# Kernel tuning notes

Hardware: AMD Instinct MI355X
Metric: run time of the kernel (lower is better)

The kernel has to match this reference:

```python
import jax, jax.numpy as jnp
import numpy as np

E = 16          # num_expert
CAP = 1024


def setup_inputs() -> dict:
    key = jax.random.key(0)
    k1, k2, k3, k4 = jax.random.split(key, 4)
    B, L, D_in, D_out, S = 2, 4096, 1024, 4096, 512
    inp = jax.random.normal(k1, (B, L, D_in), jnp.float32)
    # counts must sum to B*L; use a balanced assignment (tokens pre-sorted by expert)
    fwd_expert_count = jnp.full((E,), (B * L) // E, dtype=jnp.int32)
    weight = jax.random.normal(k2, (E, D_out, D_in), jnp.float32) * (1.0 / np.sqrt(D_in))
    bias = jax.random.normal(k3, (E, D_out), jnp.float32) * 0.02
    components = jax.random.normal(k4, (E, S, D_out), jnp.float32) * (1.0 / np.sqrt(D_out))
    return {"inp": inp, "fwd_expert_count": fwd_expert_count, "weight": weight,
            "bias": bias, "components": components}


def _forward(inp, fwd_expert_count, weight, bias, components):
    flat = inp.reshape(-1, inp.shape[-1])            # [T, D_in]
    T = flat.shape[0]
    n_exp = fwd_expert_count.shape[0]
    counts = fwd_expert_count.astype(jnp.int32)
    # per-token expert id and position within its expert segment (tokens are
    # contiguous per expert, matching fastmoe's dispatch layout)
    expert_ids = jnp.repeat(jnp.arange(n_exp, dtype=jnp.int32), counts,
                            total_repeat_length=T)                    # [T]
    offsets = jnp.concatenate([jnp.zeros((1,), jnp.int32), jnp.cumsum(counts)])
    pos = jnp.arange(T, dtype=jnp.int32) - offsets[expert_ids]        # [T]
    # scatter tokens into a padded [E, CAP, D_in] buffer (static capacity)
    padded = jnp.zeros((n_exp, CAP, flat.shape[-1]), flat.dtype)
    padded = padded.at[expert_ids, pos].set(flat)
    # grouped expert GEMM: y_e = x_e @ W_e^T + b_e  (padded rows never read back)
    y = jnp.einsum('eci,eoi->eco', padded, weight) + bias[:, None, :]  # [E, CAP, D_out]
    # projection onto components (einsum 'nkd,ksd->nks' in padded layout)
    proj = jnp.einsum('ecd,esd->ecs', y, components)                   # [E, CAP, S]
    # gather real tokens back (the upscale_proj branch in the source is dead code:
    # its result is never used in the returned output)
    out = proj[expert_ids, pos]                                        # [T, S]
    return out.reshape(inp.shape[:-1] + (proj.shape[-1],))


def reference(inp, fwd_expert_count, weight, bias, components):
    return _forward(inp, fwd_expert_count, weight, bias, components)
```

## Files before the change

kernel.cpp:

```cpp
#include <hip/hip_runtime.h>


#define NEXP 16
#define TTOK 8192
#define DIN  1024
#define DOUT 4096
#define SDIM 512
#define LDSS 40

typedef short short8 __attribute__((ext_vector_type(8)));
typedef float floatx4 __attribute__((ext_vector_type(4)));
typedef unsigned short ushort_t;

__device__ __forceinline__ ushort_t f2bf(float f) {
    union { float f; unsigned u; } v; v.f = f;
    unsigned r = v.u + 0x7FFFu + ((v.u >> 16) & 1u);
    return (ushort_t)(r >> 16);
}

__device__ __forceinline__ unsigned cvtpk(float lo, float hi) {
    unsigned r;
    asm("v_cvt_pk_bf16_f32 %0, %1, %2" : "=v"(r) : "v"(lo), "v"(hi));
    return r;
}

#define GLL16(g, l) __builtin_amdgcn_global_load_lds( \
    (const __attribute__((address_space(1))) void*)(g), \
    (__attribute__((address_space(3))) void*)(l), 16, 0, 0)

__global__ __launch_bounds__(256)
void cvt_kernel(const float* __restrict__ src, ushort_t* __restrict__ dst, int n8) {
    const int i = blockIdx.x * 256 + threadIdx.x;
    if (i >= n8) return;
    const float4 a = ((const float4*)src)[2 * i];
    const float4 b = ((const float4*)src)[2 * i + 1];
    short8 o;
    o[0] = (short)f2bf(a.x); o[1] = (short)f2bf(a.y);
    o[2] = (short)f2bf(a.z); o[3] = (short)f2bf(a.w);
    o[4] = (short)f2bf(b.x); o[5] = (short)f2bf(b.y);
    o[6] = (short)f2bf(b.z); o[7] = (short)f2bf(b.w);
    ((short8*)dst)[i] = o;
}

template<bool G1>
__global__ __launch_bounds__(512, 2)
void gemm8p(const ushort_t* __restrict__ Ain, const int* __restrict__ counts,
            const float* __restrict__ Bf, const float* __restrict__ bias,
            ushort_t* __restrict__ Yout, float* __restrict__ Pout) {
    __shared__ __align__(16) ushort_t As[2 * 16384];
    __shared__ __align__(16) ushort_t Bs[2 * 16384];

    int e, mt, nt, kq;
    if constexpr (G1) {
        const int l = ((blockIdx.x & 7) << 6) | (blockIdx.x >> 3);
        e = l >> 5; nt = (l >> 1) & 15; mt = l & 1; kq = 0;
    } else {
        const int l = ((blockIdx.x & 7) << 5) | (blockIdx.x >> 3);
        e = l >> 4; kq = (l >> 2) & 3; nt = (l >> 1) & 1; mt = l & 1;
    }
    const int LDK = G1 ? DIN : DOUT;

    int off = 0;
    for (int i = 0; i < e; ++i) off += counts[i];
    const int cnt = counts[e];

    const int tid = threadIdx.x, wave = tid >> 6, lane = tid & 63;
    const int wm = wave >> 2, wn = wave & 3;
    const int l15 = lane & 15, quad = lane >> 4;
    const int srow = (wave << 3) + (lane >> 3);
    const int swz8 = ((lane & 7) ^ (lane >> 3)) << 3;
    const int aseg = off + (mt << 8);

    const ushort_t* ap[4];
    #pragma unroll
    for (int q = 0; q < 4; ++q) {
        int r = aseg + (q << 6) + srow; if (r >= TTOK) r = TTOK - 1;
        ap[q] = Ain + (size_t)r * LDK + (G1 ? 0 : (kq << 10)) + swz8;
    }
    const float* bpq[4];
    {
        const float* Bbase = G1
            ? (Bf + (size_t)e * DOUT * DIN  + ((size_t)(nt << 8)) * DIN)
            : (Bf + (size_t)e * SDIM * DOUT + ((size_t)(nt << 8)) * DOUT + (kq << 10));
        #pragma unroll
        for (int q = 0; q < 4; ++q)
            bpq[q] = Bbase + (size_t)((q << 6) + srow) * LDK + ((lane & 7) << 3);
    }
    const int aLdsW  = (wave << 9);
    const int bWrOff = (srow << 6) + swz8;

    auto rdA = [&](int bufe, int m, int s) -> short8 {
        return *(const short8*)&As[bufe + ((wm << 7) + (m << 4) + l15) * 64
                                   + ((((s << 2) | quad) ^ (lane & 7)) << 3)];
    };
    auto rdB = [&](int bufe, int n, int s) -> short8 {
        return *(const short8*)&Bs[bufe + ((wn << 6) + (n << 4) + l15) * 64
                                   + ((((s << 2) | quad) ^ (lane & 7)) << 3)];
    };

    floatx4 acc[8][4] = {};
    short8 bfv[4][2], af0[2], af1[2];
    float4 bq[4][2];

#define GA(NB, q, kt) GLL16(ap[q] + ((kt) << 6), As + (NB) + ((q) << 12) + aLdsW)
#define LB(q, kt) { const float* _p = bpq[q] + ((kt) << 6); \
    bq[q][0] = *(const float4*)_p; bq[q][1] = *(const float4*)(_p + 4); }
#define WRB(NB, q) { uint4 _w; \
    _w.x = cvtpk(bq[q][0].x, bq[q][0].y); _w.y = cvtpk(bq[q][0].z, bq[q][0].w); \
    _w.z = cvtpk(bq[q][1].x, bq[q][1].y); _w.w = cvtpk(bq[q][1].z, bq[q][1].w); \
    *(uint4*)&Bs[(NB) + ((q) << 12) + bWrOff] = _w; }
#define RDB_ALL(BUFE) { _Pragma("unroll") \
    for (int n = 0; n < 4; ++n) { bfv[n][0] = rdB(BUFE,n,0); bfv[n][1] = rdB(BUFE,n,1); } }
#define RDA2(BUFE, M0) { af0[0]=rdA(BUFE,M0,0); af0[1]=rdA(BUFE,M0,1); \
                         af1[0]=rdA(BUFE,(M0)+1,0); af1[1]=rdA(BUFE,(M0)+1,1); }
#define MFMA16(M0) { \
    __builtin_amdgcn_s_setprio(1); \
    _Pragma("unroll") for (int n = 0; n < 4; ++n) { \
      acc[M0][n]     = __builtin_amdgcn_mfma_f32_16x16x32_bf16(af0[0], bfv[n][0], acc[M0][n],     0,0,0); \
      acc[M0][n]     = __builtin_amdgcn_mfma_f32_16x16x32_bf16(af0[1], bfv[n][1], acc[M0][n],     0,0,0); \
      acc[(M0)+1][n] = __builtin_amdgcn_mfma_f32_16x16x32_bf16(af1[0], bfv[n][0], acc[(M0)+1][n], 0,0,0); \
      acc[(M0)+1][n] = __builtin_amdgcn_mfma_f32_16x16x32_bf16(af1[1], bfv[n][1], acc[(M0)+1][n], 0,0,0); } \
    __builtin_amdgcn_s_setprio(0); }
#define VMC(N) asm volatile("s_waitcnt vmcnt(" #N ")" ::: "memory")
#define LGKM0  asm volatile("s_waitcnt lgkmcnt(0)" ::: "memory")
#define BAR()  __builtin_amdgcn_s_barrier()

#define TILE(BUF, NBUF, KA, KB) { \
    RDB_ALL(BUF); RDA2(BUF, 0); \
    GA(NBUF, 0, KA); GA(NBUF, 1, KA); \
    VMC(6); WRB(NBUF, 0); WRB(NBUF, 1); \
    LGKM0; BAR(); MFMA16(0); BAR(); \
    RDA2(BUF, 2); \
    GA(NBUF, 2, KA); GA(NBUF, 3, KA); \
    VMC(4); WRB(NBUF, 2); WRB(NBUF, 3); \
    LGKM0; BAR(); MFMA16(2); BAR(); \
    RDA2(BUF, 4); \
    LB(0, KB); LB(1, KB); \
    BAR(); MFMA16(4); BAR(); \
    RDA2(BUF, 6); \
    LB(2, KB); LB(3, KB); \
    VMC(8); \
    BAR(); MFMA16(6); BAR(); }

    LB(0, 0); LB(1, 0); LB(2, 0); LB(3, 0);
    GA(0, 0, 0); GA(0, 1, 0); GA(0, 2, 0); GA(0, 3, 0);
    VMC(4);
    WRB(0, 0); WRB(0, 1); WRB(0, 2); WRB(0, 3);
    LB(0, 1); LB(1, 1); LB(2, 1); LB(3, 1);
    VMC(8);
    LGKM0; BAR();

    #pragma unroll 1
    for (int it = 0; it < 8; ++it) {
        const int ka0 = 2 * it + 1;
        const int kb0 = (it < 7) ? 2 * it + 2 : 15;
        const int kb1 = (it < 7) ? 2 * it + 3 : 15;
        TILE(0, 16384, ka0, kb0);
        TILE(16384, 0, kb0, kb1);
    }

#undef TILE
#undef GA
#undef LB
#undef WRB
#undef RDB_ALL
#undef RDA2
#undef MFMA16
#undef VMC
#undef LGKM0
#undef BAR

    if constexpr (G1) {
        float bv[4];
        #pragma unroll
        for (int n = 0; n < 4; ++n)
            bv[n] = bias[e * DOUT + (nt << 8) + (wn << 6) + (n << 4) + l15];
        #pragma unroll
        for (int m = 0; m < 8; ++m) {
            #pragma unroll
            for (int rg = 0; rg < 4; ++rg) {
                const int trow = (mt << 8) + (wm << 7) + (m << 4) + (quad << 2) + rg;
                if (trow < cnt) {
                    ushort_t* yp = Yout + (size_t)(off + trow) * DOUT + (nt << 8) + (wn << 6);
                    #pragma unroll
                    for (int n = 0; n < 4; ++n)
                        yp[(n << 4) + l15] = f2bf(acc[m][n][rg] + bv[n]);
                }
            }
        }
    } else {
        float* pp = Pout + (size_t)kq * ((size_t)TTOK * SDIM);
        #pragma unroll
        for (int m = 0; m < 8; ++m) {
            #pragma unroll
            for (int rg = 0; rg < 4; ++rg) {
                const int trow = (mt << 8) + (wm << 7) + (m << 4) + (quad << 2) + rg;
                if (trow < cnt) {
                    float* op = pp + (size_t)(off + trow) * SDIM + (nt << 8) + (wn << 6);
                    #pragma unroll
                    for (int n = 0; n < 4; ++n)
                        op[(n << 4) + l15] = acc[m][n][rg];
                }
            }
        }
    }
}

__global__ __launch_bounds__(256)
void reduce4_kernel(const float* __restrict__ P, float* __restrict__ O) {
    const int i = blockIdx.x * 256 + threadIdx.x;
    const size_t S = (size_t)TTOK * SDIM;
    const float4 a = ((const float4*)P)[i];
    const float4 b = ((const float4*)(P + S))[i];
    const float4 c = ((const float4*)(P + 2 * S))[i];
    const float4 d = ((const float4*)(P + 3 * S))[i];
    ((float4*)O)[i] = make_float4(a.x + b.x + c.x + d.x, a.y + b.y + c.y + d.y,
                                  a.z + b.z + c.z + d.z, a.w + b.w + c.w + d.w);
}

__global__ __launch_bounds__(256, 2)
void gemm1_o(const float* __restrict__ X, const int* __restrict__ counts,
             const float* __restrict__ W, const float* __restrict__ bias,
             ushort_t* __restrict__ Y) {
    __shared__ __align__(16) ushort_t As[128 * LDSS];
    __shared__ __align__(16) ushort_t Bs[128 * LDSS];
    const int bid = blockIdx.x;
    const int e = bid >> 7, r_ = bid & 127;
    const int n_tile = r_ >> 2, m_tile = r_ & 3;
    int off = 0;
    for (int i = 0; i < e; ++i) off += counts[i];
    const int cnt = counts[e];
    const int t = threadIdx.x, wave = t >> 6, lane = t & 63;
    const int wm = (wave & 1) << 6, wn = (wave >> 1) << 6;
    const int l15 = lane & 15, quad = lane >> 4;
    const float* Wp = W + (size_t)e * DOUT * DIN + (size_t)(n_tile << 7) * DIN;
    floatx4 acc[4][4] = {};
    const int srow = t >> 3, scol = (t & 7) << 2;
    for (int k0 = 0; k0 < DIN; k0 += 32) {
        #pragma unroll
        for (int p = 0; p < 4; ++p) {
            const int row = srow + (p << 5);
            int grow = off + (m_tile << 7) + row;
            if (grow >= TTOK) grow = 0;
            const float4 v = *(const float4*)(X + (size_t)grow * DIN + k0 + scol);
            unsigned lo = (unsigned)f2bf(v.x) | ((unsigned)f2bf(v.y) << 16);
            unsigned hi = (unsigned)f2bf(v.z) | ((unsigned)f2bf(v.w) << 16);
            *(uint2*)&As[row * LDSS + scol] = make_uint2(lo, hi);
        }
        #pragma unroll
        for (int p = 0; p < 4; ++p) {
            const int row = srow + (p << 5);
            const float4 v = *(const float4*)(Wp + (size_t)row * DIN + k0 + scol);
            unsigned lo = (unsigned)f2bf(v.x) | ((unsigned)f2bf(v.y) << 16);
            unsigned hi = (unsigned)f2bf(v.z) | ((unsigned)f2bf(v.w) << 16);
            *(uint2*)&Bs[row * LDSS + scol] = make_uint2(lo, hi);
        }
        __syncthreads();
        short8 af[4], bfr[4];
        #pragma unroll
        for (int i = 0; i < 4; ++i) {
            af[i]  = *(const short8*)&As[(wm + (i << 4) + l15) * LDSS + (quad << 3)];
            bfr[i] = *(const short8*)&Bs[(wn + (i << 4) + l15) * LDSS + (quad << 3)];
        }
        #pragma unroll
        for (int mi = 0; mi < 4; ++mi)
            #pragma unroll
            for (int ni = 0; ni < 4; ++ni)
                acc[mi][ni] = __builtin_amdgcn_mfma_f32_16x16x32_bf16(
                    af[mi], bfr[ni], acc[mi][ni], 0, 0, 0);
        __syncthreads();
    }
    float bv[4];
    #pragma unroll
    for (int ni = 0; ni < 4; ++ni)
        bv[ni] = bias[e * DOUT + (n_tile << 7) + wn + (ni << 4) + l15];
    #pragma unroll
    for (int mi = 0; mi < 4; ++mi)
        #pragma unroll
        for (int rg = 0; rg < 4; ++rg) {
            const int trow = (m_tile << 7) + wm + (mi << 4) + (quad << 2) + rg;
            if (trow < cnt) {
                ushort_t* yp = Y + (size_t)(off + trow) * DOUT + (n_tile << 7) + wn;
                #pragma unroll
                for (int ni = 0; ni < 4; ++ni)
                    yp[(ni << 4) + l15] = f2bf(acc[mi][ni][rg] + bv[ni]);
            }
        }
}

__global__ __launch_bounds__(256, 2)
void gemm2_o(const ushort_t* __restrict__ Y, const int* __restrict__ counts,
             const float* __restrict__ C, float* __restrict__ O) {
    __shared__ __align__(16) ushort_t As[128 * LDSS];
    __shared__ __align__(16) ushort_t Bs[128 * LDSS];
    const int bid = blockIdx.x;
    const int e = bid >> 4, r_ = bid & 15;
    const int n_tile = r_ >> 2, m_tile = r_ & 3;
    int off = 0;
    for (int i = 0; i < e; ++i) off += counts[i];
    const int cnt = counts[e];
    const int t = threadIdx.x, wave = t >> 6, lane = t & 63;
    const int wm = (wave & 1) << 6, wn = (wave >> 1) << 6;
    const int l15 = lane & 15, quad = lane >> 4;
    const float* Cp = C + (size_t)e * SDIM * DOUT + (size_t)(n_tile << 7) * DOUT;
    floatx4 acc[4][4] = {};
    const int arow = t >> 2, achk = (t & 3) << 3;
    const int srow = t >> 3, scol = (t & 7) << 2;
    for (int k0 = 0; k0 < DOUT; k0 += 32) {
        #pragma unroll
        for (int p = 0; p < 2; ++p) {
            const int row = arow + (p << 6);
            int grow = off + (m_tile << 7) + row;
            if (grow >= TTOK) grow = 0;
            const short8 v = *(const short8*)(Y + (size_t)grow * DOUT + k0 + achk);
            *(short8*)&As[row * LDSS + achk] = v;
        }
        #pragma unroll
        for (int p = 0; p < 4; ++p) {
            const int row = srow + (p << 5);
            const float4 v = *(const float4*)(Cp + (size_t)row * DOUT + k0 + scol);
            unsigned lo = (unsigned)f2bf(v.x) | ((unsigned)f2bf(v.y) << 16);
            unsigned hi = (unsigned)f2bf(v.z) | ((unsigned)f2bf(v.w) << 16);
            *(uint2*)&Bs[row * LDSS + scol] = make_uint2(lo, hi);
        }
        __syncthreads();
        short8 af[4], bfr[4];
        #pragma unroll
        for (int i = 0; i < 4; ++i) {
            af[i]  = *(const short8*)&As[(wm + (i << 4) + l15) * LDSS + (quad << 3)];
            bfr[i] = *(const short8*)&Bs[(wn + (i << 4) + l15) * LDSS + (quad << 3)];
        }
        #pragma unroll
        for (int mi = 0; mi < 4; ++mi)
            #pragma unroll
            for (int ni = 0; ni < 4; ++ni)
                acc[mi][ni] = __builtin_amdgcn_mfma_f32_16x16x32_bf16(
                    af[mi], bfr[ni], acc[mi][ni], 0, 0, 0);
        __syncthreads();
    }
    #pragma unroll
    for (int mi = 0; mi < 4; ++mi)
        #pragma unroll
        for (int rg = 0; rg < 4; ++rg) {
            const int trow = (m_tile << 7) + wm + (mi << 4) + (quad << 2) + rg;
            if (trow < cnt) {
                float* op = O + (size_t)(off + trow) * SDIM + (n_tile << 7) + wn;
                #pragma unroll
                for (int ni = 0; ni < 4; ++ni)
                    op[(ni << 4) + l15] = acc[mi][ni][rg];
            }
        }
}

extern "C" void kernel_launch(void* const* d_in, const int* in_sizes, int n_in,
                              void* d_out, int out_size, void* d_ws, size_t ws_size,
                              hipStream_t stream) {
    const float* X      = (const float*)d_in[0];
    const int*   counts = (const int*)d_in[1];
    const float* W      = (const float*)d_in[2];
    const float* bias   = (const float*)d_in[3];
    const float* comp   = (const float*)d_in[4];
    float* out = (float*)d_out;

    const size_t OFF_XB = 0;
    const size_t OFF_Y  = 16777216;
    const size_t OFF_P  = 83886080;
    const size_t NEED   = 150994944;

    if (ws_size >= NEED) {
        ushort_t* Xb = (ushort_t*)((char*)d_ws + OFF_XB);
        ushort_t* Y  = (ushort_t*)((char*)d_ws + OFF_Y);
        float*    P  = (float*)((char*)d_ws + OFF_P);

        cvt_kernel<<<dim3(4096), dim3(256), 0, stream>>>(X, Xb, 1048576);
        gemm8p<true><<<dim3(512),  dim3(512), 0, stream>>>(Xb, counts, W, bias, Y, nullptr);
        gemm8p<false><<<dim3(256), dim3(512), 0, stream>>>(Y, counts, comp, nullptr, nullptr, P);
        reduce4_kernel<<<dim3(4096), dim3(256), 0, stream>>>(P, out);
    } else {
        ushort_t* Y = (ushort_t*)d_ws;
        gemm1_o<<<dim3(2048), dim3(256), 0, stream>>>(X, counts, W, bias, Y);
        gemm2_o<<<dim3(256),  dim3(256), 0, stream>>>(Y, counts, comp, out);
    }
}
```

Measured before the change: 566.3 us.

## Retile second GEMM to split-K by 2 with narrower N tiles

The second GEMM now splits K into 2 chunks of 2048 instead of 4 chunks of 1024, and uses 128-wide N tiles instead of 256-wide ones, with a dedicated kernel and a half-size B buffer in LDS. The partial-sum buffer shrinks from 4 to 2 slices, so the reduction kernel reads half as much data and the workspace requirement drops. The trade-off is a longer K loop per block and lower MFMA work per A-tile load, because the same A tile is now reused across fewer N columns.

```diff
diff --git a/kernel.cpp b/kernel.cpp
--- a/kernel.cpp
+++ b/kernel.cpp
@@ -42,23 +42,20 @@
     ((short8*)dst)[i] = o;
 }
 
-template<bool G1>
+#define VMC(N) asm volatile("s_waitcnt vmcnt(" #N ")" ::: "memory")
+#define LGKM0  asm volatile("s_waitcnt lgkmcnt(0)" ::: "memory")
+#define BAR()  __builtin_amdgcn_s_barrier()
+
 __global__ __launch_bounds__(512, 2)
-void gemm8p(const ushort_t* __restrict__ Ain, const int* __restrict__ counts,
-            const float* __restrict__ Bf, const float* __restrict__ bias,
-            ushort_t* __restrict__ Yout, float* __restrict__ Pout) {
+void gemm1_8p(const ushort_t* __restrict__ Ain, const int* __restrict__ counts,
+              const float* __restrict__ Bf, const float* __restrict__ bias,
+              ushort_t* __restrict__ Yout) {
     __shared__ __align__(16) ushort_t As[2 * 16384];
     __shared__ __align__(16) ushort_t Bs[2 * 16384];
 
-    int e, mt, nt, kq;
-    if constexpr (G1) {
-        const int l = ((blockIdx.x & 7) << 6) | (blockIdx.x >> 3);
-        e = l >> 5; nt = (l >> 1) & 15; mt = l & 1; kq = 0;
-    } else {
-        const int l = ((blockIdx.x & 7) << 5) | (blockIdx.x >> 3);
-        e = l >> 4; kq = (l >> 2) & 3; nt = (l >> 1) & 1; mt = l & 1;
-    }
-    const int LDK = G1 ? DIN : DOUT;
+    const int l = ((blockIdx.x & 7) << 6) | (blockIdx.x >> 3);
+    const int e = l >> 5;
+    const int nt = (l >> 1) & 15, mt = l & 1;
 
     int off = 0;
     for (int i = 0; i < e; ++i) off += counts[i];
@@ -75,16 +72,14 @@
     #pragma unroll
     for (int q = 0; q < 4; ++q) {
         int r = aseg + (q << 6) + srow; if (r >= TTOK) r = TTOK - 1;
-        ap[q] = Ain + (size_t)r * LDK + (G1 ? 0 : (kq << 10)) + swz8;
+        ap[q] = Ain + (size_t)r * DIN + swz8;
     }
     const float* bpq[4];
     {
-        const float* Bbase = G1
-            ? (Bf + (size_t)e * DOUT * DIN  + ((size_t)(nt << 8)) * DIN)
-            : (Bf + (size_t)e * SDIM * DOUT + ((size_t)(nt << 8)) * DOUT + (kq << 10));
+        const float* Bbase = Bf + (size_t)e * DOUT * DIN + ((size_t)(nt << 8)) * DIN;
         #pragma unroll
         for (int q = 0; q < 4; ++q)
-            bpq[q] = Bbase + (size_t)((q << 6) + srow) * LDK + ((lane & 7) << 3);
+            bpq[q] = Bbase + (size_t)((q << 6) + srow) * DIN + ((lane & 7) << 3);
     }
     const int aLdsW  = (wave << 9);
     const int bWrOff = (srow << 6) + swz8;
@@ -121,11 +116,8 @@
       acc[(M0)+1][n] = __builtin_amdgcn_mfma_f32_16x16x32_bf16(af1[0], bfv[n][0], acc[(M0)+1][n], 0,0,0); \
       acc[(M0)+1][n] = __builtin_amdgcn_mfma_f32_16x16x32_bf16(af1[1], bfv[n][1], acc[(M0)+1][n], 0,0,0); } \
     __builtin_amdgcn_s_setprio(0); }
-#define VMC(N) asm volatile("s_waitcnt vmcnt(" #N ")" ::: "memory")
-#define LGKM0  asm volatile("s_waitcnt lgkmcnt(0)" ::: "memory")
-#define BAR()  __builtin_amdgcn_s_barrier()
-
-#define TILE(BUF, NBUF, KA, KB) { \
+
+#define TILE1(BUF, NBUF, KA, KB) { \
     RDB_ALL(BUF); RDA2(BUF, 0); \
     GA(NBUF, 0, KA); GA(NBUF, 1, KA); \
     VMC(6); WRB(NBUF, 0); WRB(NBUF, 1); \
@@ -155,67 +147,175 @@
         const int ka0 = 2 * it + 1;
         const int kb0 = (it < 7) ? 2 * it + 2 : 15;
         const int kb1 = (it < 7) ? 2 * it + 3 : 15;
-        TILE(0, 16384, ka0, kb0);
-        TILE(16384, 0, kb0, kb1);
-    }
-
-#undef TILE
+        TILE1(0, 16384, ka0, kb0);
+        TILE1(16384, 0, kb0, kb1);
+    }
+    asm volatile("s_waitcnt vmcnt(0)" ::: "memory");
+
+#undef TILE1
 #undef GA
 #undef LB
 #undef WRB
 #undef RDB_ALL
 #undef RDA2
 #undef MFMA16
-#undef VMC
-#undef LGKM0
-#undef BAR
-
-    if constexpr (G1) {
-        float bv[4];
-        #pragma unroll
-        for (int n = 0; n < 4; ++n)
-            bv[n] = bias[e * DOUT + (nt << 8) + (wn << 6) + (n << 4) + l15];
-        #pragma unroll
-        for (int m = 0; m < 8; ++m) {
-            #pragma unroll
-            for (int rg = 0; rg < 4; ++rg) {
-                const int trow = (mt << 8) + (wm << 7) + (m << 4) + (quad << 2) + rg;
-                if (trow < cnt) {
-                    ushort_t* yp = Yout + (size_t)(off + trow) * DOUT + (nt << 8) + (wn << 6);
-                    #pragma unroll
-                    for (int n = 0; n < 4; ++n)
-                        yp[(n << 4) + l15] = f2bf(acc[m][n][rg] + bv[n]);
-                }
+
+    float bv[4];
+    #pragma unroll
+    for (int n = 0; n < 4; ++n)
+        bv[n] = bias[e * DOUT + (nt << 8) + (wn << 6) + (n << 4) + l15];
+    #pragma unroll
+    for (int m = 0; m < 8; ++m) {
+        #pragma unroll
+        for (int rg = 0; rg < 4; ++rg) {
+            const int trow = (mt << 8) + (wm << 7) + (m << 4) + (quad << 2) + rg;
+            if (trow < cnt) {
+                ushort_t* yp = Yout + (size_t)(off + trow) * DOUT + (nt << 8) + (wn << 6);
+                #pragma unroll
+                for (int n = 0; n < 4; ++n)
+                    yp[(n << 4) + l15] = f2bf(acc[m][n][rg] + bv[n]);
             }
         }
-    } else {
-        float* pp = Pout + (size_t)kq * ((size_t)TTOK * SDIM);
-        #pragma unroll
-        for (int m = 0; m < 8; ++m) {
-            #pragma unroll
-            for (int rg = 0; rg < 4; ++rg) {
-                const int trow = (mt << 8) + (wm << 7) + (m << 4) + (quad << 2) + rg;
-                if (trow < cnt) {
-                    float* op = pp + (size_t)(off + trow) * SDIM + (nt << 8) + (wn << 6);
-                    #pragma unroll
-                    for (int n = 0; n < 4; ++n)
-                        op[(n << 4) + l15] = acc[m][n][rg];
-                }
+    }
+}
+
+__global__ __launch_bounds__(512, 2)
+void gemm2_8p(const ushort_t* __restrict__ Yin, const int* __restrict__ counts,
+              const float* __restrict__ comp, float* __restrict__ P) {
+    __shared__ __align__(16) ushort_t As[2 * 16384];
+    __shared__ __align__(16) ushort_t Bs[2 * 8192];
+
+    const int l = ((blockIdx.x & 7) << 5) | (blockIdx.x >> 3);
+    const int e = l >> 4;
+    const int r = l & 15;
+    const int mt = r & 1, nt2 = (r >> 1) & 3, kq = r >> 3;
+
+    int off = 0;
+    for (int i = 0; i < e; ++i) off += counts[i];
+    const int cnt = counts[e];
+
+    const int tid = threadIdx.x, wave = tid >> 6, lane = tid & 63;
+    const int wm = wave >> 2, wn = wave & 3;
+    const int l15 = lane & 15, quad = lane >> 4;
+    const int srow = (wave << 3) + (lane >> 3);
+    const int swz8 = ((lane & 7) ^ (lane >> 3)) << 3;
+
+    const ushort_t* ap[4];
+    #pragma unroll
+    for (int q = 0; q < 4; ++q) {
+        int rr = off + (mt << 8) + (q << 6) + srow; if (rr >= TTOK) rr = TTOK - 1;
+        ap[q] = Yin + (size_t)rr * DOUT + (kq << 11) + swz8;
+    }
+    const float* bph[2];
+    {
+        const float* Bbase = comp + (size_t)e * SDIM * DOUT
+                           + ((size_t)(nt2 << 7)) * DOUT + (kq << 11);
+        #pragma unroll
+        for (int h = 0; h < 2; ++h)
+            bph[h] = Bbase + (size_t)((h << 6) + srow) * DOUT + ((lane & 7) << 3);
+    }
+    const int aLdsW  = (wave << 9);
+    const int bWrOff = (srow << 6) + swz8;
+
+    auto rdA = [&](int bufe, int m, int s) -> short8 {
+        return *(const short8*)&As[bufe + ((wm << 7) + (m << 4) + l15) * 64
+                                   + ((((s << 2) | quad) ^ (lane & 7)) << 3)];
+    };
+    auto rdB = [&](int bufe, int n, int s) -> short8 {
+        return *(const short8*)&Bs[bufe + ((wn << 5) + (n << 4) + l15) * 64
+                                   + ((((s << 2) | quad) ^ (lane & 7)) << 3)];
+    };
+
+    floatx4 acc[8][2] = {};
+    short8 bfv[2][2], af0[2], af1[2];
+    float4 bq[2][2];
+
+#define GA2(AB, q, kt) GLL16(ap[q] + ((kt) << 6), As + (AB) + ((q) << 12) + aLdsW)
+#define LB2(h, kt) { const float* _p = bph[h] + ((kt) << 6); \
+    bq[h][0] = *(const float4*)_p; bq[h][1] = *(const float4*)(_p + 4); }
+#define WRB2(BB, h) { uint4 _w; \
+    _w.x = cvtpk(bq[h][0].x, bq[h][0].y); _w.y = cvtpk(bq[h][0].z, bq[h][0].w); \
+    _w.z = cvtpk(bq[h][1].x, bq[h][1].y); _w.w = cvtpk(bq[h][1].z, bq[h][1].w); \
+    *(uint4*)&Bs[(BB) + ((h) << 12) + bWrOff] = _w; }
+#define RDB_ALL2(BB) { _Pragma("unroll") \
+    for (int n = 0; n < 2; ++n) { bfv[n][0] = rdB(BB,n,0); bfv[n][1] = rdB(BB,n,1); } }
+#define RDA2(AB, M0) { af0[0]=rdA(AB,M0,0); af0[1]=rdA(AB,M0,1); \
+                       af1[0]=rdA(AB,(M0)+1,0); af1[1]=rdA(AB,(M0)+1,1); }
+#define MFMA8(M0) { \
+    __builtin_amdgcn_s_setprio(1); \
+    _Pragma("unroll") for (int n = 0; n < 2; ++n) { \
+      acc[M0][n]     = __builtin_amdgcn_mfma_f32_16x16x32_bf16(af0[0], bfv[n][0], acc[M0][n],     0,0,0); \
+      acc[M0][n]     = __builtin_amdgcn_mfma_f32_16x16x32_bf16(af0[1], bfv[n][1], acc[M0][n],     0,0,0); \
+      acc[(M0)+1][n] = __builtin_amdgcn_mfma_f32_16x16x32_bf16(af1[0], bfv[n][0], acc[(M0)+1][n], 0,0,0); \
+      acc[(M0)+1][n] = __builtin_amdgcn_mfma_f32_16x16x32_bf16(af1[1], bfv[n][1], acc[(M0)+1][n], 0,0,0); } \
+    __builtin_amdgcn_s_setprio(0); }
+
+#define TILE2(AB, BB, NAB, NBB, KA, KB) { \
+    RDB_ALL2(BB); RDA2(AB, 0); \
+    GA2(NAB, 0, KA); GA2(NAB, 1, KA); \
+    VMC(4); WRB2(NBB, 0); \
+    LGKM0; BAR(); MFMA8(0); BAR(); \
+    RDA2(AB, 2); \
+    GA2(NAB, 2, KA); GA2(NAB, 3, KA); \
+    VMC(4); WRB2(NBB, 1); \
+    LGKM0; BAR(); MFMA8(2); BAR(); \
+    RDA2(AB, 4); \
+    LB2(0, KB); \
+    BAR(); MFMA8(4); BAR(); \
+    RDA2(AB, 6); \
+    LB2(1, KB); \
+    VMC(4); \
+    BAR(); MFMA8(6); BAR(); }
+
+    LB2(0, 0); LB2(1, 0);
+    GA2(0, 0, 0); GA2(0, 1, 0); GA2(0, 2, 0); GA2(0, 3, 0);
+    VMC(4);
+    WRB2(0, 0); WRB2(0, 1);
+    LB2(0, 1); LB2(1, 1);
+    VMC(4);
+    LGKM0; BAR();
+
+    #pragma unroll 1
+    for (int it = 0; it < 16; ++it) {
+        const int ka0 = 2 * it + 1;
+        const int kb0 = (it < 15) ? 2 * it + 2 : 31;
+        const int kb1 = (it < 15) ? 2 * it + 3 : 31;
+        TILE2(0, 0, 16384, 8192, ka0, kb0);
+        TILE2(16384, 8192, 0, 0, kb0, kb1);
+    }
+    asm volatile("s_waitcnt vmcnt(0)" ::: "memory");
+
+#undef TILE2
+#undef GA2
+#undef LB2
+#undef WRB2
+#undef RDB_ALL2
+#undef RDA2
+#undef MFMA8
+
+    float* pp = P + (size_t)kq * ((size_t)TTOK * SDIM);
+    #pragma unroll
+    for (int m = 0; m < 8; ++m) {
+        #pragma unroll
+        for (int rg = 0; rg < 4; ++rg) {
+            const int trow = (mt << 8) + (wm << 7) + (m << 4) + (quad << 2) + rg;
+            if (trow < cnt) {
+                float* op = pp + (size_t)(off + trow) * SDIM + (nt2 << 7) + (wn << 5);
+                #pragma unroll
+                for (int n = 0; n < 2; ++n)
+                    op[(n << 4) + l15] = acc[m][n][rg];
             }
         }
     }
 }
 
 __global__ __launch_bounds__(256)
-void reduce4_kernel(const float* __restrict__ P, float* __restrict__ O) {
+void reduce2_kernel(const float* __restrict__ P, float* __restrict__ O) {
     const int i = blockIdx.x * 256 + threadIdx.x;
     const size_t S = (size_t)TTOK * SDIM;
     const float4 a = ((const float4*)P)[i];
     const float4 b = ((const float4*)(P + S))[i];
-    const float4 c = ((const float4*)(P + 2 * S))[i];
-    const float4 d = ((const float4*)(P + 3 * S))[i];
-    ((float4*)O)[i] = make_float4(a.x + b.x + c.x + d.x, a.y + b.y + c.y + d.y,
-                                  a.z + b.z + c.z + d.z, a.w + b.w + c.w + d.w);
+    ((float4*)O)[i] = make_float4(a.x + b.x, a.y + b.y, a.z + b.z, a.w + b.w);
 }
 
 __global__ __launch_bounds__(256, 2)
@@ -365,7 +465,7 @@
     const size_t OFF_XB = 0;
     const size_t OFF_Y  = 16777216;
     const size_t OFF_P  = 83886080;
-    const size_t NEED   = 150994944;
+    const size_t NEED   = 117440512;
 
     if (ws_size >= NEED) {
         ushort_t* Xb = (ushort_t*)((char*)d_ws + OFF_XB);
@@ -373,9 +473,9 @@
         float*    P  = (float*)((char*)d_ws + OFF_P);
 
         cvt_kernel<<<dim3(4096), dim3(256), 0, stream>>>(X, Xb, 1048576);
-        gemm8p<true><<<dim3(512),  dim3(512), 0, stream>>>(Xb, counts, W, bias, Y, nullptr);
-        gemm8p<false><<<dim3(256), dim3(512), 0, stream>>>(Y, counts, comp, nullptr, nullptr, P);
-        reduce4_kernel<<<dim3(4096), dim3(256), 0, stream>>>(P, out);
+        gemm1_8p<<<dim3(512), dim3(512), 0, stream>>>(Xb, counts, W, bias, Y);
+        gemm2_8p<<<dim3(256), dim3(512), 0, stream>>>(Y, counts, comp, P);
+        reduce2_kernel<<<dim3(4096), dim3(256), 0, stream>>>(P, out);
     } else {
         ushort_t* Y = (ushort_t*)d_ws;
         gemm1_o<<<dim3(2048), dim3(256), 0, stream>>>(X, counts, W, bias, Y);
```

New measurement: 571.8 us. About the same (+1.0%).
